# Performance work log

Measured on AMD Instinct MI355X. Metric: run time of the kernel, lower is better.

The kernel has to match this reference:

```python
import jax, jax.numpy as jnp
import numpy as np

D_MODEL = 1024
N_HEADS = 16
D_KEY = D_MODEL // N_HEADS


def setup_inputs() -> dict:
    key = jax.random.key(0)
    ks = jax.random.split(key, 11)
    s = 1.0 / np.sqrt(D_MODEL)
    inp = {
        'query': jax.random.normal(ks[0], (2, 2048, D_MODEL), dtype=jnp.float32),
        'key': jax.random.normal(ks[1], (2, 2048, D_MODEL), dtype=jnp.float32),
        'value': jax.random.normal(ks[2], (2, 2048, D_MODEL), dtype=jnp.float32),
        'Wq': jax.random.uniform(ks[3], (D_MODEL, D_MODEL), jnp.float32, -s, s),
        'bq': jax.random.uniform(ks[4], (D_MODEL,), jnp.float32, -s, s),
        'Wk': jax.random.uniform(ks[5], (D_MODEL, D_MODEL), jnp.float32, -s, s),
        'bk': jax.random.uniform(ks[6], (D_MODEL,), jnp.float32, -s, s),
        'Wv': jax.random.uniform(ks[7], (D_MODEL, D_MODEL), jnp.float32, -s, s),
        'bv': jax.random.uniform(ks[8], (D_MODEL,), jnp.float32, -s, s),
        'Wo': jax.random.uniform(ks[9], (D_MODEL, D_MODEL), jnp.float32, -s, s),
        'bo': jax.random.uniform(ks[10], (D_MODEL,), jnp.float32, -s, s),
    }
    return inp


def _split_heads(x):
    b, s, _ = x.shape
    return x.reshape(b, s, N_HEADS, D_KEY).transpose(0, 2, 1, 3)  # [b,h,s,dk]


def reference(query, key, value, Wq, bq, Wk, bk, Wv, bv, Wo, bo):
    q = _split_heads(query @ Wq.T + bq)
    k = _split_heads(key @ Wk.T + bk)
    v = _split_heads(value @ Wv.T + bv)
    scale = 1.0 / jnp.sqrt(jnp.float32(D_KEY))
    scores = jnp.einsum('bhqd,bhkd->bhqk', q, k) * scale  # [b,h,s,s]
    probs = jax.nn.softmax(scores, axis=-1)
    attn = jnp.einsum('bhqk,bhkd->bhqd', probs, v)
    b, h, s, dk = attn.shape
    combined = attn.transpose(0, 2, 1, 3).reshape(b, s, D_MODEL)
    return combined @ Wo.T + bo
```

## Files before the change

### kernel.cpp

```cpp
#include <hip/hip_runtime.h>
#include <hip/hip_bf16.h>

#define DEVI __device__ __forceinline__

typedef short bf16x8 __attribute__((ext_vector_type(8)));
typedef float f32x4  __attribute__((ext_vector_type(4)));

#define WS_XQ   0u
#define WS_XK   4194304u
#define WS_XV   8388608u
#define WS_WQ   12582912u
#define WS_WK   13631488u
#define WS_WV   14680064u
#define WS_WO   15728640u
#define WS_QB   16777216u
#define WS_KB   20971520u
#define WS_VT   25165824u
#define WS_CB   29360128u

#define QSCALE 0.18033688011112042f

DEVI short f2bf(float f) {
  union { float f; unsigned u; } c; c.f = f;
  return (short)((c.u + 0x8000u) >> 16);
}

DEVI unsigned pk2(float a, float b) {
  union { float f; unsigned u; } x, y; x.f = a; y.f = b;
  return ((x.u + 0x8000u) >> 16) | ((y.u + 0x8000u) & 0xffff0000u);
}

DEVI void async16(const short* g, const short* l) {
  __builtin_amdgcn_global_load_lds(
      (const __attribute__((address_space(1))) void*)g,
      (__attribute__((address_space(3))) void*)l, 16, 0, 0);
}

__global__ __launch_bounds__(256) void conv_kernel(
    const float* __restrict__ q, const float* __restrict__ k, const float* __restrict__ v,
    const float* __restrict__ Wq, const float* __restrict__ Wk,
    const float* __restrict__ Wv, const float* __restrict__ Wo,
    short* __restrict__ ws)
{
  size_t e = ((size_t)blockIdx.x * 256 + threadIdx.x) * 8;
  const float* src; short* dst; float sc = 1.0f;
  if (e < 12582912u) {
    size_t which = e >> 22;
    size_t off   = e & 4194303u;
    src = (which == 0 ? q : which == 1 ? k : v) + off;
    dst = ws + which * 4194304u + off;
  } else {
    size_t j = e - 12582912u;
    size_t which = j >> 20;
    size_t off   = j & 1048575u;
    src = (which == 0 ? Wq : which == 1 ? Wk : which == 2 ? Wv : Wo) + off;
    dst = ws + 12582912u + which * 1048576u + off;
    if (which == 0) sc = QSCALE;
  }
  float4 f0 = *(const float4*)src;
  float4 f1 = *(const float4*)(src + 4);
  int4 o;
  o.x = pk2(f0.x * sc, f0.y * sc);
  o.y = pk2(f0.z * sc, f0.w * sc);
  o.z = pk2(f1.x * sc, f1.y * sc);
  o.w = pk2(f1.z * sc, f1.w * sc);
  *(int4*)dst = o;
}

template <int BN>
DEVI void gemm_body(const short* __restrict__ A, const short* __restrict__ Bt,
                    const float* __restrict__ bias, void* __restrict__ C,
                    int outmode, float bscale)
{
  constexpr int Kd = 1024, Nd = 1024;
  constexpr int NT = BN / 32;
  constexpr int BI = BN / 32;
  __shared__ __attribute__((aligned(16))) short smem[8192 + BN * 64];
  short* As = smem;
  short* Bs = smem + 8192;

  const int tid  = threadIdx.x;
  const int lane = tid & 63;
  const int w    = tid >> 6;
  const int quad = lane >> 4, cl = lane & 15;
  const int m0 = blockIdx.y * 128, n0 = blockIdx.x * BN;
  const int wm = (w >> 1) * 64, wn = (w & 1) * (BN / 2);

  f32x4 acc[4][NT];
#pragma unroll
  for (int i = 0; i < 4; ++i)
#pragma unroll
    for (int j = 0; j < NT; ++j)
#pragma unroll
      for (int r = 0; r < 4; ++r) acc[i][j][r] = 0.0f;

  for (int k0 = 0; k0 < Kd; k0 += 64) {
    __syncthreads();
#pragma unroll
    for (int i = 0; i < 4; ++i) {
      int ubase = (w * 4 + i) * 64;
      int f = ubase + lane;
      int r = f >> 3;
      int kb = (f & 7) ^ (r & 7);
      async16(A + (size_t)(m0 + r) * Kd + k0 + kb * 8, As + ubase * 8);
    }
#pragma unroll
    for (int i = 0; i < BI; ++i) {
      int ubase = (w * BI + i) * 64;
      int f = ubase + lane;
      int r = f >> 3;
      int kb = (f & 7) ^ (r & 7);
      async16(Bt + (size_t)(n0 + r) * Kd + k0 + kb * 8, Bs + ubase * 8);
    }
    __builtin_amdgcn_s_waitcnt(0);
    __syncthreads();

#pragma unroll
    for (int ks = 0; ks < 2; ++ks) {
      bf16x8 af[4], bfr[NT];
#pragma unroll
      for (int mt = 0; mt < 4; ++mt) {
        int r = wm + mt * 16 + cl;
        int u = (r << 3) | (((ks << 2) | quad) ^ (r & 7));
        af[mt] = *(const bf16x8*)&As[u * 8];
      }
#pragma unroll
      for (int nt = 0; nt < NT; ++nt) {
        int r = wn + nt * 16 + cl;
        int u = (r << 3) | (((ks << 2) | quad) ^ (r & 7));
        bfr[nt] = *(const bf16x8*)&Bs[u * 8];
      }
#pragma unroll
      for (int mt = 0; mt < 4; ++mt)
#pragma unroll
        for (int nt = 0; nt < NT; ++nt)
          acc[mt][nt] = __builtin_amdgcn_mfma_f32_16x16x32_bf16(af[mt], bfr[nt], acc[mt][nt], 0, 0, 0);
    }
  }

  if (BN == 128 && outmode == 1) {
    __syncthreads();
#pragma unroll
    for (int mt = 0; mt < 4; ++mt)
#pragma unroll
      for (int nt = 0; nt < NT; ++nt) {
        int n_l = wn + nt * 16 + cl;
        float bv = bias[n0 + n_l] * bscale;
        int m_base = wm + mt * 16 + quad * 4;
        short4 pk;
        pk.x = f2bf(acc[mt][nt][0] + bv);
        pk.y = f2bf(acc[mt][nt][1] + bv);
        pk.z = f2bf(acc[mt][nt][2] + bv);
        pk.w = f2bf(acc[mt][nt][3] + bv);
        int u = m_base >> 2;
        int addr = n_l * 128 + ((u ^ (n_l & 31)) << 2);
        *(short4*)&smem[addr] = pk;
      }
    __syncthreads();
    short* Cs = (short*)C;
    int bb = m0 >> 11;
    int s0 = m0 & 2047;
#pragma unroll
    for (int p = 0; p < 4; ++p) {
      int n_l = w * 32 + p * 8 + (lane >> 3);
      int mb = (lane & 7) * 16;
      short4 t0, t1, t2, t3;
      {
        int u = (mb >> 2) + 0; t0 = *(short4*)&smem[n_l * 128 + ((u ^ (n_l & 31)) << 2)];
        u = (mb >> 2) + 1;     t1 = *(short4*)&smem[n_l * 128 + ((u ^ (n_l & 31)) << 2)];
        u = (mb >> 2) + 2;     t2 = *(short4*)&smem[n_l * 128 + ((u ^ (n_l & 31)) << 2)];
        u = (mb >> 2) + 3;     t3 = *(short4*)&smem[n_l * 128 + ((u ^ (n_l & 31)) << 2)];
      }
      size_t g = ((size_t)(bb * 1024 + n0 + n_l)) * 2048 + s0 + mb;
      *(short4*)&Cs[g]      = t0;
      *(short4*)&Cs[g + 4]  = t1;
      *(short4*)&Cs[g + 8]  = t2;
      *(short4*)&Cs[g + 12] = t3;
    }
    return;
  }

#pragma unroll
  for (int mt = 0; mt < 4; ++mt)
#pragma unroll
    for (int nt = 0; nt < NT; ++nt) {
      int n = n0 + wn + nt * 16 + cl;
      float bv = bias[n] * bscale;
#pragma unroll
      for (int r = 0; r < 4; ++r) {
        int m = m0 + wm + mt * 16 + quad * 4 + r;
        float val = acc[mt][nt][r] + bv;
        if (outmode == 2) ((float*)C)[(size_t)m * Nd + n] = val;
        else              ((short*)C)[(size_t)m * Nd + n] = f2bf(val);
      }
    }
}

__global__ __launch_bounds__(256) void proj_gemm(
    short* ws, const float* __restrict__ bq, const float* __restrict__ bk,
    const float* __restrict__ bv)
{
  int z = blockIdx.z;
  const short* A; const short* W; const float* bias; void* C;
  int mode; float bscale = 1.0f;
  if (z == 0)      { A = ws + WS_XQ; W = ws + WS_WQ; bias = bq; C = ws + WS_QB; mode = 0; bscale = QSCALE; }
  else if (z == 1) { A = ws + WS_XK; W = ws + WS_WK; bias = bk; C = ws + WS_KB; mode = 0; }
  else             { A = ws + WS_XV; W = ws + WS_WV; bias = bv; C = ws + WS_VT; mode = 1; }
  gemm_body<128>(A, W, bias, C, mode, bscale);
}

__global__ __launch_bounds__(256) void out_gemm(
    const short* __restrict__ ws, const float* __restrict__ bo, float* __restrict__ out)
{
  gemm_body<64>(ws + WS_CB, ws + WS_WO, bo, out, 2, 1.0f);
}

__global__ __launch_bounds__(256, 2) void flash_kernel(
    const short* __restrict__ Qb, const short* __restrict__ Kb,
    const short* __restrict__ Vt, short* __restrict__ comb)
{
  __shared__ __attribute__((aligned(16))) short QsPs[8192];
  __shared__ __attribute__((aligned(16))) short Ks[3][4096];
  __shared__ __attribute__((aligned(16))) short Vts[3][4096];

  const int tid = threadIdx.x, lane = tid & 63, w = tid >> 6;
  const int quad = lane >> 4, cl = lane & 15;
  const int b = blockIdx.z, h = blockIdx.y, q0 = blockIdx.x * 128;
  const int qrow_base = w * 32;

  const short* Qg = Qb + ((size_t)(b * 2048 + q0)) * 1024 + h * 64;
  const short* Kg = Kb + ((size_t)(b * 2048)) * 1024 + h * 64;
  const short* Vg = Vt + ((size_t)(b * 1024 + h * 64)) * 2048;

  auto stageKV = [&](int j0, short* Kd, short* Vd) {
#pragma unroll
    for (int i = 0; i < 2; ++i) {
      int ubase = (w * 2 + i) * 64;
      int f = ubase + lane;
      int r = f >> 3, kb = (f & 7) ^ (r & 7);
      async16(Kg + (size_t)(j0 + r) * 1024 + kb * 8, Kd + ubase * 8);
      async16(Vg + (size_t)r * 2048 + j0 + kb * 8, Vd + ubase * 8);
    }
  };

#pragma unroll
  for (int i = 0; i < 4; ++i) {
    int ubase = (w * 4 + i) * 64;
    int f = ubase + lane;
    int r = f >> 3, kb = (f & 7) ^ (r & 7);
    async16(Qg + (size_t)r * 1024 + kb * 8, QsPs + ubase * 8);
  }
  stageKV(0, Ks[0], Vts[0]);
  stageKV(64, Ks[1], Vts[1]);
  __builtin_amdgcn_s_waitcnt(0);

  bf16x8 qa[2][2];
#pragma unroll
  for (int qt = 0; qt < 2; ++qt)
#pragma unroll
    for (int ks = 0; ks < 2; ++ks) {
      int r = qrow_base + qt * 16 + cl;
      int off = r * 64 + ((((ks << 2) | quad) ^ (r & 7)) << 3);
      qa[qt][ks] = *(const bf16x8*)&QsPs[off];
    }
  __syncthreads();

  auto qk = [&](const short* Kc, f32x4 (&dst)[4][2]) {
#pragma unroll
    for (int m = 0; m < 4; ++m)
#pragma unroll
      for (int qt = 0; qt < 2; ++qt)
#pragma unroll
        for (int r = 0; r < 4; ++r) dst[m][qt][r] = 0.0f;
#pragma unroll
    for (int ks = 0; ks < 2; ++ks) {
      bf16x8 ka[4];
#pragma unroll
      for (int m = 0; m < 4; ++m) {
        int r = m * 16 + cl;
        int off = r * 64 + ((((ks << 2) | quad) ^ (r & 7)) << 3);
        ka[m] = *(const bf16x8*)&Kc[off];
      }
#pragma unroll
      for (int m = 0; m < 4; ++m)
#pragma unroll
        for (int qt = 0; qt < 2; ++qt)
          dst[m][qt] = __builtin_amdgcn_mfma_f32_16x16x32_bf16(ka[m], qa[qt][ks], dst[m][qt], 0, 0, 0);
    }
  };

  f32x4 sA[4][2], sB[4][2];
  f32x4 accO[2][4];
  f32x4 accL[2];
#pragma unroll
  for (int qt = 0; qt < 2; ++qt) {
#pragma unroll
    for (int r = 0; r < 4; ++r) accL[qt][r] = 0.0f;
#pragma unroll
    for (int d = 0; d < 4; ++d)
#pragma unroll
      for (int r = 0; r < 4; ++r) accO[qt][d][r] = 0.0f;
  }

  const bf16x8 ones = { 0x3F80, 0x3F80, 0x3F80, 0x3F80, 0x3F80, 0x3F80, 0x3F80, 0x3F80 };

  qk(Ks[0], sA);

  auto body = [&](int j, f32x4 (&cur)[4][2], f32x4 (&nxt)[4][2]) {
    if (j + 2 < 32) {
      int bi = (j + 2) % 3;
      stageKV((j + 2) * 64, Ks[bi], Vts[bi]);
    }
    if (j + 1 < 32) qk(Ks[(j + 1) % 3], nxt);
#pragma unroll
    for (int ksub = 0; ksub < 4; ++ksub)
#pragma unroll
      for (int qt = 0; qt < 2; ++qt) {
        int qrow = qrow_base + qt * 16 + cl;
        int u = ksub * 2 + (quad >> 1);
        int off = qrow * 64 + ((u ^ (qrow & 7)) << 3) + ((quad & 1) << 2);
        int2 pk;
        pk.x = pk2(__builtin_amdgcn_exp2f(cur[ksub][qt][0]),
                   __builtin_amdgcn_exp2f(cur[ksub][qt][1]));
        pk.y = pk2(__builtin_amdgcn_exp2f(cur[ksub][qt][2]),
                   __builtin_amdgcn_exp2f(cur[ksub][qt][3]));
        *(int2*)&QsPs[off] = pk;
      }
    const short* Vc = Vts[j % 3];
#pragma unroll
    for (int kt = 0; kt < 2; ++kt) {
      bf16x8 pa[2];
#pragma unroll
      for (int qt = 0; qt < 2; ++qt) {
        int qrow = qrow_base + qt * 16 + cl;
        int off = qrow * 64 + ((((kt << 2) | quad) ^ (qrow & 7)) << 3);
        pa[qt] = *(const bf16x8*)&QsPs[off];
        accL[qt] = __builtin_amdgcn_mfma_f32_16x16x32_bf16(pa[qt], ones, accL[qt], 0, 0, 0);
      }
#pragma unroll
      for (int d = 0; d < 4; ++d) {
        int r = d * 16 + cl;
        int off = r * 64 + ((((kt << 2) | quad) ^ (r & 7)) << 3);
        bf16x8 vb = *(const bf16x8*)&Vc[off];
#pragma unroll
        for (int qt = 0; qt < 2; ++qt)
          accO[qt][d] = __builtin_amdgcn_mfma_f32_16x16x32_bf16(pa[qt], vb, accO[qt][d], 0, 0, 0);
      }
    }
    __builtin_amdgcn_s_waitcnt(0);
    __syncthreads();
  };

  for (int j = 0; j < 32; j += 2) {
    body(j, sA, sB);
    body(j + 1, sB, sA);
  }

#pragma unroll
  for (int qt = 0; qt < 2; ++qt) {
    float inv[4];
#pragma unroll
    for (int r = 0; r < 4; ++r) inv[r] = 1.0f / accL[qt][r];
#pragma unroll
    for (int d = 0; d < 4; ++d)
#pragma unroll
      for (int r = 0; r < 4; ++r) {
        int q = q0 + qrow_base + qt * 16 + quad * 4 + r;
        int dc = d * 16 + cl;
        comb[((size_t)(b * 2048 + q)) * 1024 + h * 64 + dc] = f2bf(accO[qt][d][r] * inv[r]);
      }
  }
}

extern "C" void kernel_launch(void* const* d_in, const int* in_sizes, int n_in,
                              void* d_out, int out_size, void* d_ws, size_t ws_size,
                              hipStream_t stream) {
  const float* q  = (const float*)d_in[0];
  const float* k  = (const float*)d_in[1];
  const float* v  = (const float*)d_in[2];
  const float* Wq = (const float*)d_in[3];
  const float* bq = (const float*)d_in[4];
  const float* Wk = (const float*)d_in[5];
  const float* bk = (const float*)d_in[6];
  const float* Wv = (const float*)d_in[7];
  const float* bv = (const float*)d_in[8];
  const float* Wo = (const float*)d_in[9];
  const float* bo = (const float*)d_in[10];
  short* ws = (short*)d_ws;
  float* out = (float*)d_out;

  conv_kernel<<<8192, 256, 0, stream>>>(q, k, v, Wq, Wk, Wv, Wo, ws);
  proj_gemm<<<dim3(8, 32, 3), 256, 0, stream>>>(ws, bq, bk, bv);
  flash_kernel<<<dim3(16, 16, 2), 256, 0, stream>>>(ws + WS_QB, ws + WS_KB, ws + WS_VT, ws + WS_CB);
  out_gemm<<<dim3(16, 32), 256, 0, stream>>>(ws, bo, out);
}
```

Baseline: 227.0 us.

## Double-buffer GEMM k-tiles and shrink flash KV tiles for higher occupancy

The projection and output GEMMs now stage 32-wide K tiles into two LDS buffers, prefetching the next tile while the current one is multiplied. This replaces the single-buffer load-then-compute loop with its two barriers per step, and uses a new 4-chunk XOR swizzle. The flash kernel halves its KV tile to 32 keys with smaller K/V ring buffers, and launch bounds request more blocks per CU, trading more loop iterations and barriers for higher occupancy and latency hiding.

```diff
diff --git a/kernel.cpp b/kernel.cpp
--- a/kernel.cpp
+++ b/kernel.cpp
@@ -74,10 +74,7 @@
 {
   constexpr int Kd = 1024, Nd = 1024;
   constexpr int NT = BN / 32;
-  constexpr int BI = BN / 32;
-  __shared__ __attribute__((aligned(16))) short smem[8192 + BN * 64];
-  short* As = smem;
-  short* Bs = smem + 8192;
+  __shared__ __attribute__((aligned(16))) short smem[2][4096 + BN * 32];
 
   const int tid  = threadIdx.x;
   const int lane = tid & 63;
@@ -86,6 +83,25 @@
   const int m0 = blockIdx.y * 128, n0 = blockIdx.x * BN;
   const int wm = (w >> 1) * 64, wn = (w & 1) * (BN / 2);
 
+  auto stage = [&](int k0, int buf) {
+    short* Ab = &smem[buf][0];
+    short* Bb = &smem[buf][4096];
+#pragma unroll
+    for (int i = 0; i < 2; ++i) {
+      int f = (w * 2 + i) * 64 + lane;
+      int r = f >> 2;
+      int kb = (f & 3) ^ (r & 3) ^ ((r >> 2) & 1);
+      async16(A + (size_t)(m0 + r) * Kd + k0 + kb * 8, Ab + f * 8);
+    }
+#pragma unroll
+    for (int i = 0; i < BN / 64; ++i) {
+      int f = (w * (BN / 64) + i) * 64 + lane;
+      int r = f >> 2;
+      int kb = (f & 3) ^ (r & 3) ^ ((r >> 2) & 1);
+      async16(Bt + (size_t)(n0 + r) * Kd + k0 + kb * 8, Bb + f * 8);
+    }
+  };
+
   f32x4 acc[4][NT];
 #pragma unroll
   for (int i = 0; i < 4; ++i)
@@ -94,52 +110,38 @@
 #pragma unroll
       for (int r = 0; r < 4; ++r) acc[i][j][r] = 0.0f;
 
-  for (int k0 = 0; k0 < Kd; k0 += 64) {
-    __syncthreads();
-#pragma unroll
-    for (int i = 0; i < 4; ++i) {
-      int ubase = (w * 4 + i) * 64;
-      int f = ubase + lane;
-      int r = f >> 3;
-      int kb = (f & 7) ^ (r & 7);
-      async16(A + (size_t)(m0 + r) * Kd + k0 + kb * 8, As + ubase * 8);
-    }
-#pragma unroll
-    for (int i = 0; i < BI; ++i) {
-      int ubase = (w * BI + i) * 64;
-      int f = ubase + lane;
-      int r = f >> 3;
-      int kb = (f & 7) ^ (r & 7);
-      async16(Bt + (size_t)(n0 + r) * Kd + k0 + kb * 8, Bs + ubase * 8);
-    }
+  stage(0, 0);
+  __builtin_amdgcn_s_waitcnt(0);
+  __syncthreads();
+
+  for (int j = 0; j < 32; ++j) {
+    if (j < 31) stage((j + 1) * 32, (j + 1) & 1);
+    const short* Ab = &smem[j & 1][0];
+    const short* Bb = &smem[j & 1][4096];
+    bf16x8 af[4], bfr[NT];
+#pragma unroll
+    for (int mt = 0; mt < 4; ++mt) {
+      int r = wm + mt * 16 + cl;
+      int off = r * 32 + ((quad ^ (r & 3) ^ ((r >> 2) & 1)) << 3);
+      af[mt] = *(const bf16x8*)&Ab[off];
+    }
+#pragma unroll
+    for (int nt = 0; nt < NT; ++nt) {
+      int r = wn + nt * 16 + cl;
+      int off = r * 32 + ((quad ^ (r & 3) ^ ((r >> 2) & 1)) << 3);
+      bfr[nt] = *(const bf16x8*)&Bb[off];
+    }
+#pragma unroll
+    for (int mt = 0; mt < 4; ++mt)
+#pragma unroll
+      for (int nt = 0; nt < NT; ++nt)
+        acc[mt][nt] = __builtin_amdgcn_mfma_f32_16x16x32_bf16(af[mt], bfr[nt], acc[mt][nt], 0, 0, 0);
     __builtin_amdgcn_s_waitcnt(0);
     __syncthreads();
-
-#pragma unroll
-    for (int ks = 0; ks < 2; ++ks) {
-      bf16x8 af[4], bfr[NT];
-#pragma unroll
-      for (int mt = 0; mt < 4; ++mt) {
-        int r = wm + mt * 16 + cl;
-        int u = (r << 3) | (((ks << 2) | quad) ^ (r & 7));
-        af[mt] = *(const bf16x8*)&As[u * 8];
-      }
-#pragma unroll
-      for (int nt = 0; nt < NT; ++nt) {
-        int r = wn + nt * 16 + cl;
-        int u = (r << 3) | (((ks << 2) | quad) ^ (r & 7));
-        bfr[nt] = *(const bf16x8*)&Bs[u * 8];
-      }
-#pragma unroll
-      for (int mt = 0; mt < 4; ++mt)
-#pragma unroll
-        for (int nt = 0; nt < NT; ++nt)
-          acc[mt][nt] = __builtin_amdgcn_mfma_f32_16x16x32_bf16(af[mt], bfr[nt], acc[mt][nt], 0, 0, 0);
-    }
   }
 
   if (BN == 128 && outmode == 1) {
-    __syncthreads();
+    short* flat = &smem[0][0];
 #pragma unroll
     for (int mt = 0; mt < 4; ++mt)
 #pragma unroll
@@ -154,7 +156,7 @@
         pk.w = f2bf(acc[mt][nt][3] + bv);
         int u = m_base >> 2;
         int addr = n_l * 128 + ((u ^ (n_l & 31)) << 2);
-        *(short4*)&smem[addr] = pk;
+        *(short4*)&flat[addr] = pk;
       }
     __syncthreads();
     short* Cs = (short*)C;
@@ -166,10 +168,10 @@
       int mb = (lane & 7) * 16;
       short4 t0, t1, t2, t3;
       {
-        int u = (mb >> 2) + 0; t0 = *(short4*)&smem[n_l * 128 + ((u ^ (n_l & 31)) << 2)];
-        u = (mb >> 2) + 1;     t1 = *(short4*)&smem[n_l * 128 + ((u ^ (n_l & 31)) << 2)];
-        u = (mb >> 2) + 2;     t2 = *(short4*)&smem[n_l * 128 + ((u ^ (n_l & 31)) << 2)];
-        u = (mb >> 2) + 3;     t3 = *(short4*)&smem[n_l * 128 + ((u ^ (n_l & 31)) << 2)];
+        int u = (mb >> 2) + 0; t0 = *(short4*)&flat[n_l * 128 + ((u ^ (n_l & 31)) << 2)];
+        u = (mb >> 2) + 1;     t1 = *(short4*)&flat[n_l * 128 + ((u ^ (n_l & 31)) << 2)];
+        u = (mb >> 2) + 2;     t2 = *(short4*)&flat[n_l * 128 + ((u ^ (n_l & 31)) << 2)];
+        u = (mb >> 2) + 3;     t3 = *(short4*)&flat[n_l * 128 + ((u ^ (n_l & 31)) << 2)];
       }
       size_t g = ((size_t)(bb * 1024 + n0 + n_l)) * 2048 + s0 + mb;
       *(short4*)&Cs[g]      = t0;
@@ -196,7 +198,7 @@
     }
 }
 
-__global__ __launch_bounds__(256) void proj_gemm(
+__global__ __launch_bounds__(256, 3) void proj_gemm(
     short* ws, const float* __restrict__ bq, const float* __restrict__ bk,
     const float* __restrict__ bv)
 {
@@ -209,19 +211,19 @@
   gemm_body<128>(A, W, bias, C, mode, bscale);
 }
 
-__global__ __launch_bounds__(256) void out_gemm(
+__global__ __launch_bounds__(256, 3) void out_gemm(
     const short* __restrict__ ws, const float* __restrict__ bo, float* __restrict__ out)
 {
   gemm_body<64>(ws + WS_CB, ws + WS_WO, bo, out, 2, 1.0f);
 }
 
-__global__ __launch_bounds__(256, 2) void flash_kernel(
+__global__ __launch_bounds__(256, 4) void flash_kernel(
     const short* __restrict__ Qb, const short* __restrict__ Kb,
     const short* __restrict__ Vt, short* __restrict__ comb)
 {
   __shared__ __attribute__((aligned(16))) short QsPs[8192];
-  __shared__ __attribute__((aligned(16))) short Ks[3][4096];
-  __shared__ __attribute__((aligned(16))) short Vts[3][4096];
+  __shared__ __attribute__((aligned(16))) short Ks[3][2048];
+  __shared__ __attribute__((aligned(16))) short Vts[2][2048];
 
   const int tid = threadIdx.x, lane = tid & 63, w = tid >> 6;
   const int quad = lane >> 4, cl = lane & 15;
@@ -232,26 +234,28 @@
   const short* Kg = Kb + ((size_t)(b * 2048)) * 1024 + h * 64;
   const short* Vg = Vt + ((size_t)(b * 1024 + h * 64)) * 2048;
 
-  auto stageKV = [&](int j0, short* Kd, short* Vd) {
-#pragma unroll
-    for (int i = 0; i < 2; ++i) {
-      int ubase = (w * 2 + i) * 64;
-      int f = ubase + lane;
-      int r = f >> 3, kb = (f & 7) ^ (r & 7);
-      async16(Kg + (size_t)(j0 + r) * 1024 + kb * 8, Kd + ubase * 8);
-      async16(Vg + (size_t)r * 2048 + j0 + kb * 8, Vd + ubase * 8);
-    }
+  auto stageK = [&](int j0, short* Kd) {
+    int f = w * 64 + lane;
+    int r = f >> 3;
+    int kb = (f & 7) ^ (r & 7);
+    async16(Kg + (size_t)(j0 + r) * 1024 + kb * 8, Kd + f * 8);
+  };
+  auto stageV = [&](int j0, short* Vd) {
+    int f = w * 64 + lane;
+    int r = f >> 2;
+    int kb = (f & 3) ^ (r & 3) ^ ((r >> 2) & 1);
+    async16(Vg + (size_t)r * 2048 + j0 + kb * 8, Vd + f * 8);
   };
 
 #pragma unroll
   for (int i = 0; i < 4; ++i) {
-    int ubase = (w * 4 + i) * 64;
-    int f = ubase + lane;
+    int f = (w * 4 + i) * 64 + lane;
     int r = f >> 3, kb = (f & 7) ^ (r & 7);
-    async16(Qg + (size_t)r * 1024 + kb * 8, QsPs + ubase * 8);
-  }
-  stageKV(0, Ks[0], Vts[0]);
-  stageKV(64, Ks[1], Vts[1]);
+    async16(Qg + (size_t)r * 1024 + kb * 8, QsPs + f * 8);
+  }
+  stageK(0, Ks[0]);
+  stageK(32, Ks[1]);
+  stageV(0, Vts[0]);
   __builtin_amdgcn_s_waitcnt(0);
 
   bf16x8 qa[2][2];
@@ -265,31 +269,31 @@
     }
   __syncthreads();
 
-  auto qk = [&](const short* Kc, f32x4 (&dst)[4][2]) {
-#pragma unroll
-    for (int m = 0; m < 4; ++m)
+  auto qk = [&](const short* Kc, f32x4 (&dst)[2][2]) {
+#pragma unroll
+    for (int m = 0; m < 2; ++m)
 #pragma unroll
       for (int qt = 0; qt < 2; ++qt)
 #pragma unroll
         for (int r = 0; r < 4; ++r) dst[m][qt][r] = 0.0f;
 #pragma unroll
     for (int ks = 0; ks < 2; ++ks) {
-      bf16x8 ka[4];
-#pragma unroll
-      for (int m = 0; m < 4; ++m) {
+      bf16x8 ka[2];
+#pragma unroll
+      for (int m = 0; m < 2; ++m) {
         int r = m * 16 + cl;
         int off = r * 64 + ((((ks << 2) | quad) ^ (r & 7)) << 3);
         ka[m] = *(const bf16x8*)&Kc[off];
       }
 #pragma unroll
-      for (int m = 0; m < 4; ++m)
+      for (int m = 0; m < 2; ++m)
 #pragma unroll
         for (int qt = 0; qt < 2; ++qt)
           dst[m][qt] = __builtin_amdgcn_mfma_f32_16x16x32_bf16(ka[m], qa[qt][ks], dst[m][qt], 0, 0, 0);
     }
   };
 
-  f32x4 sA[4][2], sB[4][2];
+  f32x4 sA[2][2], sB[2][2];
   f32x4 accO[2][4];
   f32x4 accL[2];
 #pragma unroll
@@ -306,52 +310,50 @@
 
   qk(Ks[0], sA);
 
-  auto body = [&](int j, f32x4 (&cur)[4][2], f32x4 (&nxt)[4][2]) {
-    if (j + 2 < 32) {
-      int bi = (j + 2) % 3;
-      stageKV((j + 2) * 64, Ks[bi], Vts[bi]);
-    }
-    if (j + 1 < 32) qk(Ks[(j + 1) % 3], nxt);
-#pragma unroll
-    for (int ksub = 0; ksub < 4; ++ksub)
+  int r0 = 0, r1 = 1, r2 = 2;
+  auto body = [&](int j, f32x4 (&cur)[2][2], f32x4 (&nxt)[2][2]) {
+    if (j + 2 < 64) stageK((j + 2) * 32, Ks[r2]);
+    if (j + 1 < 64) { stageV((j + 1) * 32, Vts[(j + 1) & 1]); qk(Ks[r1], nxt); }
+#pragma unroll
+    for (int m = 0; m < 2; ++m)
 #pragma unroll
       for (int qt = 0; qt < 2; ++qt) {
         int qrow = qrow_base + qt * 16 + cl;
-        int u = ksub * 2 + (quad >> 1);
-        int off = qrow * 64 + ((u ^ (qrow & 7)) << 3) + ((quad & 1) << 2);
+        int sw = (qrow & 3) ^ ((qrow >> 2) & 1);
+        int u = m * 2 + (quad >> 1);
+        int off = qrow * 32 + (((u ^ sw)) << 3) + ((quad & 1) << 2);
         int2 pk;
-        pk.x = pk2(__builtin_amdgcn_exp2f(cur[ksub][qt][0]),
-                   __builtin_amdgcn_exp2f(cur[ksub][qt][1]));
-        pk.y = pk2(__builtin_amdgcn_exp2f(cur[ksub][qt][2]),
-                   __builtin_amdgcn_exp2f(cur[ksub][qt][3]));
+        pk.x = pk2(__builtin_amdgcn_exp2f(cur[m][qt][0]),
+                   __builtin_amdgcn_exp2f(cur[m][qt][1]));
+        pk.y = pk2(__builtin_amdgcn_exp2f(cur[m][qt][2]),
+                   __builtin_amdgcn_exp2f(cur[m][qt][3]));
         *(int2*)&QsPs[off] = pk;
       }
-    const short* Vc = Vts[j % 3];
-#pragma unroll
-    for (int kt = 0; kt < 2; ++kt) {
-      bf16x8 pa[2];
-#pragma unroll
-      for (int qt = 0; qt < 2; ++qt) {
-        int qrow = qrow_base + qt * 16 + cl;
-        int off = qrow * 64 + ((((kt << 2) | quad) ^ (qrow & 7)) << 3);
-        pa[qt] = *(const bf16x8*)&QsPs[off];
-        accL[qt] = __builtin_amdgcn_mfma_f32_16x16x32_bf16(pa[qt], ones, accL[qt], 0, 0, 0);
-      }
-#pragma unroll
-      for (int d = 0; d < 4; ++d) {
-        int r = d * 16 + cl;
-        int off = r * 64 + ((((kt << 2) | quad) ^ (r & 7)) << 3);
-        bf16x8 vb = *(const bf16x8*)&Vc[off];
-#pragma unroll
-        for (int qt = 0; qt < 2; ++qt)
-          accO[qt][d] = __builtin_amdgcn_mfma_f32_16x16x32_bf16(pa[qt], vb, accO[qt][d], 0, 0, 0);
-      }
+    const short* Vc = Vts[j & 1];
+    bf16x8 pa[2];
+#pragma unroll
+    for (int qt = 0; qt < 2; ++qt) {
+      int qrow = qrow_base + qt * 16 + cl;
+      int sw = (qrow & 3) ^ ((qrow >> 2) & 1);
+      int off = qrow * 32 + ((quad ^ sw) << 3);
+      pa[qt] = *(const bf16x8*)&QsPs[off];
+      accL[qt] = __builtin_amdgcn_mfma_f32_16x16x32_bf16(pa[qt], ones, accL[qt], 0, 0, 0);
+    }
+#pragma unroll
+    for (int d = 0; d < 4; ++d) {
+      int rr = d * 16 + cl;
+      int off = rr * 32 + ((quad ^ (rr & 3) ^ ((rr >> 2) & 1)) << 3);
+      bf16x8 vb = *(const bf16x8*)&Vc[off];
+#pragma unroll
+      for (int qt = 0; qt < 2; ++qt)
+        accO[qt][d] = __builtin_amdgcn_mfma_f32_16x16x32_bf16(pa[qt], vb, accO[qt][d], 0, 0, 0);
     }
     __builtin_amdgcn_s_waitcnt(0);
     __syncthreads();
-  };
-
-  for (int j = 0; j < 32; j += 2) {
+    int t = r0; r0 = r1; r1 = r2; r2 = t;
+  };
+
+  for (int j = 0; j < 64; j += 2) {
     body(j, sA, sB);
     body(j + 1, sB, sA);
   }
```

Result: slower. 231.6 us (+2.0%).
